# Kernel optimization log

Measured on AMD Instinct MI355X. Metric: run time of the kernel, lower is better.

## Reference

```python
import math
import jax, jax.numpy as jnp
import numpy as np

SAMPLE_RATE = 16000
N_BANDS = 3
_F_DARK = jnp.array([270.0, 800.0, 2300.0], dtype=jnp.float32)
_F_NEUTRAL = jnp.array([500.0, 1500.0, 2500.0], dtype=jnp.float32)
_F_BRIGHT = jnp.array([730.0, 2100.0, 3000.0], dtype=jnp.float32)
_Q_DARK = jnp.array([5.0, 5.0, 5.0], dtype=jnp.float32)
_Q_NEUTRAL = jnp.array([8.0, 8.0, 8.0], dtype=jnp.float32)
_Q_BRIGHT = jnp.array([12.0, 12.0, 12.0], dtype=jnp.float32)


def _interpolate_formants(level):
    # level: [B] in [0,1] -> freqs, qs: [B, n_bands]
    t_low = jnp.clip(level * 2.0, 0.0, 1.0)[:, None]
    t_high = jnp.clip((level - 0.5) * 2.0, 0.0, 1.0)[:, None]
    use_high = (level >= 0.5)[:, None]
    freqs_lo = (1.0 - t_low) * _F_DARK + t_low * _F_NEUTRAL
    qs_lo = (1.0 - t_low) * _Q_DARK + t_low * _Q_NEUTRAL
    freqs_hi = (1.0 - t_high) * _F_NEUTRAL + t_high * _F_BRIGHT
    qs_hi = (1.0 - t_high) * _Q_NEUTRAL + t_high * _Q_BRIGHT
    freqs = jnp.where(use_high, freqs_hi, freqs_lo)
    qs = jnp.where(use_high, qs_hi, qs_lo)
    return freqs, qs


def _biquad_bandpass_coeffs(freq_hz, q):
    # freq_hz, q: [B, n_bands] -> coeffs each [B, n_bands]; b1 is 0
    omega = (2.0 * math.pi / SAMPLE_RATE) * freq_hz
    sin_o = jnp.sin(omega)
    cos_o = jnp.cos(omega)
    alpha = sin_o / (2.0 * jnp.maximum(q, 0.5))
    a0 = 1.0 + alpha
    b0 = alpha / a0
    b2 = -alpha / a0
    a1 = (-2.0 * cos_o) / a0
    a2 = (1.0 - alpha) / a0
    return b0, b2, a1, a2


def setup_inputs() -> dict:
    key = jax.random.key(0)
    k1, k2 = jax.random.split(key)
    B, S = 256, 131072
    audio = jax.random.normal(k1, (B, S), dtype=jnp.float32)
    resonance_level = jax.random.uniform(k2, (B,), dtype=jnp.float32)
    return {"audio": audio, "resonance_level": resonance_level}


def reference(audio, resonance_level):
    B, S = audio.shape
    level = jnp.clip(resonance_level.astype(audio.dtype), 0.0, 1.0)
    freqs, qs = _interpolate_formants(level)          # [B, nb]
    b0, b2, a1, a2 = _biquad_bandpass_coeffs(freqs, qs)
    # broadcast coeffs to [nb, B] for the scan
    b0, b2, a1, a2 = (c.T for c in (b0, b2, a1, a2))
    nb = N_BANDS
    zeros = jnp.zeros((nb, B), dtype=audio.dtype)
    inv_sqrt_nb = 1.0 / math.sqrt(nb)

    def step(carry, x_t):
        # carry: (x1, x2, y1, y2) each [nb, B]; x_t: [B]
        x1, x2, y1, y2 = carry
        y = b0 * x_t[None, :] + b2 * x2 - a1 * y1 - a2 * y2  # [nb, B]
        new_x1 = jnp.broadcast_to(x_t[None, :], (nb, B))
        return (new_x1, x1, y, y1), jnp.sum(y, axis=0) * inv_sqrt_nb

    _, out = jax.lax.scan(step, (zeros, zeros, zeros, zeros), audio.T)  # out: [S, B]
    return out.T
```

## Files before the change

kernel.cpp:

```cpp
#include <hip/hip_runtime.h>
#include <math.h>

#ifndef M_PI
#define M_PI 3.14159265358979323846
#endif

#define BATCHES 256
#define S_LEN   131072

#define TPB   320
#define MAINT 256
#define CCH   16
#define SEGS  32
#define SEG_SAMPS (MAINT * CCH)
#define WCH   48
#define NCH   (MAINT + WCH)
#define OBSTR 17
#define SCAN_OFF 4352
#define SCAN_STR 305
#define H_OFF 6184
#define LDSF  6232

typedef float v4f __attribute__((ext_vector_type(4)));

__device__ __forceinline__ void compute_coeffs(float level_in, float b0[3], float na1[3], float na2[3]) {
    const float FD[3] = {270.0f, 800.0f, 2300.0f};
    const float FN[3] = {500.0f, 1500.0f, 2500.0f};
    const float FB[3] = {730.0f, 2100.0f, 3000.0f};
    float level = fminf(fmaxf(level_in, 0.0f), 1.0f);
    float t_low  = fminf(fmaxf(level * 2.0f, 0.0f), 1.0f);
    float t_high = fminf(fmaxf((level - 0.5f) * 2.0f, 0.0f), 1.0f);
    bool hi = (level >= 0.5f);
    const float W0 = (float)(2.0 * M_PI / 16000.0);
    #pragma unroll
    for (int k = 0; k < 3; ++k) {
        float f, q;
        if (hi) { f = (1.0f - t_high) * FN[k] + t_high * FB[k];
                  q = (1.0f - t_high) * 8.0f  + t_high * 12.0f; }
        else    { f = (1.0f - t_low) * FD[k] + t_low * FN[k];
                  q = (1.0f - t_low) * 5.0f  + t_low * 8.0f; }
        float omega = W0 * f;
        float sn = __sinf(omega), cs = __cosf(omega);
        float alpha = sn / (2.0f * fmaxf(q, 0.5f));
        float a0 = 1.0f + alpha;
        b0[k]  = alpha / a0;
        na1[k] = (2.0f * cs) / a0;
        na2[k] = -((1.0f - alpha) / a0);
    }
}

#define STEP3(XT, XTM2, SUMV)                                                    \
    {                                                                            \
        float d = (XT) - (XTM2);                                                 \
        float e0 = fmaf(b0[0], d, na2[0] * y2[0]);                               \
        float e1 = fmaf(b0[1], d, na2[1] * y2[1]);                               \
        float e2 = fmaf(b0[2], d, na2[2] * y2[2]);                               \
        float yy0 = fmaf(na1[0], y1[0], e0);                                     \
        float yy1 = fmaf(na1[1], y1[1], e1);                                     \
        float yy2 = fmaf(na1[2], y1[2], e2);                                     \
        y2[0] = y1[0]; y1[0] = yy0;                                              \
        y2[1] = y1[1]; y1[1] = yy1;                                              \
        y2[2] = y1[2]; y1[2] = yy2;                                              \
        SUMV = (yy0 + yy1 + yy2);                                                \
    }

#define MMUL(R00,R01,R10,R11, X00,X01,X10,X11, Y00,Y01,Y10,Y11)                  \
    {                                                                            \
        R00 = X00*Y00 + X01*Y10; R01 = X00*Y01 + X01*Y11;                        \
        R10 = X10*Y00 + X11*Y10; R11 = X10*Y01 + X11*Y11;                        \
    }

__global__ __launch_bounds__(TPB, 2)
void formant_onepass(const float* __restrict__ x, const float* __restrict__ lvl,
                     float* __restrict__ out)
{
    __shared__ float lds[LDSF];

    const int tid = threadIdx.x;
    const int row = blockIdx.x >> 5;
    const int seg = blockIdx.x & (SEGS - 1);

    float b0[3], na1[3], na2[3];
    compute_coeffs(lvl[row], b0, na1, na2);

    const float* xrow = x + (size_t)row * S_LEN;
    const size_t segBase = (size_t)seg * SEG_SAMPS;

    if (tid < MAINT) {
        const float* xc = xrow + segBase + (size_t)tid * CCH;
        float xm1 = 0.f, xm2 = 0.f;
        if (seg > 0 || tid > 0) { float2 t2 = *(const float2*)(xc - 2); xm2 = t2.x; xm1 = t2.y; }
        float y1[3] = {0.f,0.f,0.f}, y2[3] = {0.f,0.f,0.f};
        const float4* xv = (const float4*)xc;
        float* myob = lds + tid * OBSTR;
        float4 buf[4];
        #pragma unroll
        for (int j = 0; j < 4; ++j) buf[j] = xv[j];
        #pragma unroll
        for (int i = 0; i < 4; ++i) {
            float4 q = buf[i];
            float4 o;
            STEP3(q.x, xm2, o.x)
            STEP3(q.y, xm1, o.y)
            STEP3(q.z, q.x, o.z)
            STEP3(q.w, q.y, o.w)
            xm2 = q.z; xm1 = q.w;
            myob[4*i + 0] = o.x;
            myob[4*i + 1] = o.y;
            myob[4*i + 2] = o.z;
            myob[4*i + 3] = o.w;
        }
        lds[SCAN_OFF + 0*SCAN_STR + WCH + tid] = y1[0];
        lds[SCAN_OFF + 1*SCAN_STR + WCH + tid] = y2[0];
        lds[SCAN_OFF + 2*SCAN_STR + WCH + tid] = y1[1];
        lds[SCAN_OFF + 3*SCAN_STR + WCH + tid] = y2[1];
        lds[SCAN_OFF + 4*SCAN_STR + WCH + tid] = y1[2];
        lds[SCAN_OFF + 5*SCAN_STR + WCH + tid] = y2[2];
    }
    else if (tid < MAINT + WCH) {
        const int wid = tid - MAINT;
        if (seg == 0) {
            #pragma unroll
            for (int e = 0; e < 6; ++e) lds[SCAN_OFF + e*SCAN_STR + wid] = 0.f;
        } else {
            const float* xw = xrow + segBase - (size_t)(WCH * CCH) + (size_t)wid * CCH;
            float2 t2 = *(const float2*)(xw - 2);
            float y1[3] = {0.f,0.f,0.f}, y2[3] = {0.f,0.f,0.f};
            float p2 = t2.x, p1 = t2.y, dummy;
            const float4* xv = (const float4*)xw;
            float4 buf[4];
            #pragma unroll
            for (int j = 0; j < 4; ++j) buf[j] = xv[j];
            #pragma unroll
            for (int i = 0; i < 4; ++i) {
                float4 q = buf[i];
                STEP3(q.x, p2, dummy)
                STEP3(q.y, p1, dummy)
                STEP3(q.z, q.x, dummy)
                STEP3(q.w, q.y, dummy)
                p2 = q.z; p1 = q.w;
            }
            (void)dummy;
            lds[SCAN_OFF + 0*SCAN_STR + wid] = y1[0];
            lds[SCAN_OFF + 1*SCAN_STR + wid] = y2[0];
            lds[SCAN_OFF + 2*SCAN_STR + wid] = y1[1];
            lds[SCAN_OFF + 3*SCAN_STR + wid] = y2[1];
            lds[SCAN_OFF + 4*SCAN_STR + wid] = y1[2];
            lds[SCAN_OFF + 5*SCAN_STR + wid] = y2[2];
        }
    }
    __syncthreads();

    {
        const int wv = tid >> 6, ln = tid & 63;
        if (wv < 3) {
            const float A1 = na1[wv], A2 = na2[wv];
            float hm1 = 1.f, hm2 = 0.f, hm3 = 0.f;
            for (int i = 0; i < CCH; ++i) {
                float h = fmaf(A1, hm1, A2 * hm2);
                hm3 = hm2; hm2 = hm1; hm1 = h;
                if (ln == 0) lds[H_OFF + wv * CCH + i] = h;
            }
            const float H00 = hm1, H01 = A2 * hm2;
            const float H10 = hm2, H11 = A2 * hm3;

            float* z1p = lds + SCAN_OFF + (2*wv) * SCAN_STR;
            float* z2p = lds + SCAN_OFF + (2*wv + 1) * SCAN_STR;

            const int cnt = (ln < 48) ? 5 : 4;
            const int beg = (ln < 48) ? 5 * ln : 240 + 4 * (ln - 48);

            float s1 = 0.f, s2 = 0.f;
            for (int j = 0; j < cnt; ++j) {
                float z1 = z1p[beg + j], z2 = z2p[beg + j];
                float n1 = z1 + H00 * s1 + H01 * s2;
                float n2 = z2 + H10 * s1 + H11 * s2;
                s1 = n1; s2 = n2;
            }
            float B00,B01,B10,B11, C00,C01,C10,C11;
            MMUL(B00,B01,B10,B11, H00,H01,H10,H11, H00,H01,H10,H11)
            MMUL(C00,C01,C10,C11, B00,B01,B10,B11, B00,B01,B10,B11)
            float A00 = C00, A01 = C01, A10 = C10, A11 = C11;
            if (cnt == 5) {
                float D00,D01,D10,D11;
                MMUL(D00,D01,D10,D11, C00,C01,C10,C11, H00,H01,H10,H11)
                A00 = D00; A01 = D01; A10 = D10; A11 = D11;
            }
            float bb1 = s1, bb2 = s2;
            for (int d = 1; d < 64; d <<= 1) {
                float iA00 = __shfl_up(A00, d), iA01 = __shfl_up(A01, d);
                float iA10 = __shfl_up(A10, d), iA11 = __shfl_up(A11, d);
                float ib1  = __shfl_up(bb1, d), ib2  = __shfl_up(bb2, d);
                if (ln >= d) {
                    float nb1 = A00 * ib1 + A01 * ib2 + bb1;
                    float nb2 = A10 * ib1 + A11 * ib2 + bb2;
                    float n00, n01, n10, n11;
                    MMUL(n00,n01,n10,n11, A00,A01,A10,A11, iA00,iA01,iA10,iA11)
                    A00 = n00; A01 = n01; A10 = n10; A11 = n11;
                    bb1 = nb1; bb2 = nb2;
                }
            }
            float e1 = __shfl_up(bb1, 1), e2 = __shfl_up(bb2, 1);
            if (ln == 0) { e1 = 0.f; e2 = 0.f; }

            s1 = e1; s2 = e2;
            for (int j = 0; j < cnt; ++j) {
                int w = beg + j;
                float z1 = z1p[w], z2 = z2p[w];
                z1p[w] = s1; z2p[w] = s2;
                float n1 = z1 + H00 * s1 + H01 * s2;
                float n2 = z2 + H10 * s1 + H11 * s2;
                s1 = n1; s2 = n2;
            }
        }
    }
    __syncthreads();

    {
        const float is3 = 0.57735026918962576f;
        float* obase = out + (size_t)row * S_LEN + segBase;

#define EMIT_OUT(F)                                                              \
        {                                                                        \
            const int f   = (F);                                                 \
            const int ch  = f >> 2;                                              \
            const int off = f & 3;                                               \
            const int t   = off * 4;                                             \
            const float* sp = lds + ch * OBSTR + t;                              \
            float o0 = sp[0], o1 = sp[1], o2 = sp[2], o3 = sp[3];                \
            _Pragma("unroll")                                                    \
            for (int k = 0; k < 3; ++k) {                                        \
                const float c1 = lds[SCAN_OFF + (2*k)   * SCAN_STR + WCH + ch];  \
                const float c2 = na2[k] *                                        \
                    lds[SCAN_OFF + (2*k+1) * SCAN_STR + WCH + ch];               \
                const float4 hv = *(const float4*)&lds[H_OFF + k * CCH + t];     \
                const float hm = (off == 0) ? 1.0f : lds[H_OFF + k*CCH + t - 1]; \
                o0 = fmaf(c1, hv.x, fmaf(c2, hm,   o0));                         \
                o1 = fmaf(c1, hv.y, fmaf(c2, hv.x, o1));                         \
                o2 = fmaf(c1, hv.z, fmaf(c2, hv.y, o2));                         \
                o3 = fmaf(c1, hv.w, fmaf(c2, hv.z, o3));                         \
            }                                                                    \
            v4f o = { o0 * is3, o1 * is3, o2 * is3, o3 * is3 };                  \
            __builtin_nontemporal_store(o, (v4f*)(obase + (size_t)f * 4));       \
        }

        #pragma unroll
        for (int j = 0; j < 3; ++j)
            EMIT_OUT(j * TPB + tid)
        if (tid < 1024 - 3 * TPB)
            EMIT_OUT(3 * TPB + tid)
#undef EMIT_OUT
    }
}

extern "C" void kernel_launch(void* const* d_in, const int* in_sizes, int n_in,
                              void* d_out, int out_size, void* d_ws, size_t ws_size,
                              hipStream_t stream) {
    const float* audio = (const float*)d_in[0];
    const float* level = (const float*)d_in[1];
    float* out = (float*)d_out;
    (void)in_sizes; (void)n_in; (void)d_ws; (void)ws_size; (void)out_size;

    formant_onepass<<<BATCHES * SEGS, TPB, 0, stream>>>(audio, level, out);
}
```

Before: 58.00 us.

## Keep zero-state outputs in registers and apply carry correction before LDS transpose

```diff
diff --git a/kernel.cpp b/kernel.cpp
--- a/kernel.cpp
+++ b/kernel.cpp
@@ -14,12 +14,10 @@
 #define SEGS  32
 #define SEG_SAMPS (MAINT * CCH)
 #define WCH   48
-#define NCH   (MAINT + WCH)
-#define OBSTR 17
-#define SCAN_OFF 4352
+#define OBSTR 20
 #define SCAN_STR 305
-#define H_OFF 6184
-#define LDSF  6232
+#define H_OFF 5120
+#define LDSF  (H_OFF + 3 * CCH)
 
 typedef float v4f __attribute__((ext_vector_type(4)));
 
@@ -86,13 +84,14 @@
     const float* xrow = x + (size_t)row * S_LEN;
     const size_t segBase = (size_t)seg * SEG_SAMPS;
 
+    float4 szs[4];
+
     if (tid < MAINT) {
         const float* xc = xrow + segBase + (size_t)tid * CCH;
         float xm1 = 0.f, xm2 = 0.f;
         if (seg > 0 || tid > 0) { float2 t2 = *(const float2*)(xc - 2); xm2 = t2.x; xm1 = t2.y; }
         float y1[3] = {0.f,0.f,0.f}, y2[3] = {0.f,0.f,0.f};
         const float4* xv = (const float4*)xc;
-        float* myob = lds + tid * OBSTR;
         float4 buf[4];
         #pragma unroll
         for (int j = 0; j < 4; ++j) buf[j] = xv[j];
@@ -105,23 +104,20 @@
             STEP3(q.z, q.x, o.z)
             STEP3(q.w, q.y, o.w)
             xm2 = q.z; xm1 = q.w;
-            myob[4*i + 0] = o.x;
-            myob[4*i + 1] = o.y;
-            myob[4*i + 2] = o.z;
-            myob[4*i + 3] = o.w;
-        }
-        lds[SCAN_OFF + 0*SCAN_STR + WCH + tid] = y1[0];
-        lds[SCAN_OFF + 1*SCAN_STR + WCH + tid] = y2[0];
-        lds[SCAN_OFF + 2*SCAN_STR + WCH + tid] = y1[1];
-        lds[SCAN_OFF + 3*SCAN_STR + WCH + tid] = y2[1];
-        lds[SCAN_OFF + 4*SCAN_STR + WCH + tid] = y1[2];
-        lds[SCAN_OFF + 5*SCAN_STR + WCH + tid] = y2[2];
+            szs[i] = o;
+        }
+        lds[0*SCAN_STR + WCH + tid] = y1[0];
+        lds[1*SCAN_STR + WCH + tid] = y2[0];
+        lds[2*SCAN_STR + WCH + tid] = y1[1];
+        lds[3*SCAN_STR + WCH + tid] = y2[1];
+        lds[4*SCAN_STR + WCH + tid] = y1[2];
+        lds[5*SCAN_STR + WCH + tid] = y2[2];
     }
     else if (tid < MAINT + WCH) {
         const int wid = tid - MAINT;
         if (seg == 0) {
             #pragma unroll
-            for (int e = 0; e < 6; ++e) lds[SCAN_OFF + e*SCAN_STR + wid] = 0.f;
+            for (int e = 0; e < 6; ++e) lds[e*SCAN_STR + wid] = 0.f;
         } else {
             const float* xw = xrow + segBase - (size_t)(WCH * CCH) + (size_t)wid * CCH;
             float2 t2 = *(const float2*)(xw - 2);
@@ -141,12 +137,12 @@
                 p2 = q.z; p1 = q.w;
             }
             (void)dummy;
-            lds[SCAN_OFF + 0*SCAN_STR + wid] = y1[0];
-            lds[SCAN_OFF + 1*SCAN_STR + wid] = y2[0];
-            lds[SCAN_OFF + 2*SCAN_STR + wid] = y1[1];
-            lds[SCAN_OFF + 3*SCAN_STR + wid] = y2[1];
-            lds[SCAN_OFF + 4*SCAN_STR + wid] = y1[2];
-            lds[SCAN_OFF + 5*SCAN_STR + wid] = y2[2];
+            lds[0*SCAN_STR + wid] = y1[0];
+            lds[1*SCAN_STR + wid] = y2[0];
+            lds[2*SCAN_STR + wid] = y1[1];
+            lds[3*SCAN_STR + wid] = y2[1];
+            lds[4*SCAN_STR + wid] = y1[2];
+            lds[5*SCAN_STR + wid] = y2[2];
         }
     }
     __syncthreads();
@@ -164,8 +160,8 @@
             const float H00 = hm1, H01 = A2 * hm2;
             const float H10 = hm2, H11 = A2 * hm3;
 
-            float* z1p = lds + SCAN_OFF + (2*wv) * SCAN_STR;
-            float* z2p = lds + SCAN_OFF + (2*wv + 1) * SCAN_STR;
+            float* z1p = lds + (2*wv) * SCAN_STR;
+            float* z2p = lds + (2*wv + 1) * SCAN_STR;
 
             const int cnt = (ln < 48) ? 5 : 4;
             const int beg = (ln < 48) ? 5 * ln : 240 + 4 * (ln - 48);
@@ -216,40 +212,52 @@
     }
     __syncthreads();
 
+    float c1k[3], c2k[3];
+    if (tid < MAINT) {
+        #pragma unroll
+        for (int k = 0; k < 3; ++k) {
+            c1k[k] = lds[(2*k) * SCAN_STR + WCH + tid];
+            c2k[k] = na2[k] * lds[(2*k + 1) * SCAN_STR + WCH + tid];
+        }
+    }
+    __syncthreads();
+
+    if (tid < MAINT) {
+        const float is3 = 0.57735026918962576f;
+        float* myst = lds + tid * OBSTR;
+        float hp[3] = {1.f, 1.f, 1.f};
+        #pragma unroll
+        for (int i = 0; i < 4; ++i) {
+            float4 s = szs[i];
+            float o0 = s.x, o1 = s.y, o2 = s.z, o3 = s.w;
+            #pragma unroll
+            for (int k = 0; k < 3; ++k) {
+                const float4 hv = *(const float4*)&lds[H_OFF + k * CCH + 4 * i];
+                o0 = fmaf(c1k[k], hv.x, fmaf(c2k[k], hp[k], o0));
+                o1 = fmaf(c1k[k], hv.y, fmaf(c2k[k], hv.x,  o1));
+                o2 = fmaf(c1k[k], hv.z, fmaf(c2k[k], hv.y,  o2));
+                o3 = fmaf(c1k[k], hv.w, fmaf(c2k[k], hv.z,  o3));
+                hp[k] = hv.w;
+            }
+            v4f o = { o0 * is3, o1 * is3, o2 * is3, o3 * is3 };
+            *(v4f*)(myst + 4 * i) = o;
+        }
+    }
+    __syncthreads();
+
     {
-        const float is3 = 0.57735026918962576f;
         float* obase = out + (size_t)row * S_LEN + segBase;
-
-#define EMIT_OUT(F)                                                              \
-        {                                                                        \
-            const int f   = (F);                                                 \
-            const int ch  = f >> 2;                                              \
-            const int off = f & 3;                                               \
-            const int t   = off * 4;                                             \
-            const float* sp = lds + ch * OBSTR + t;                              \
-            float o0 = sp[0], o1 = sp[1], o2 = sp[2], o3 = sp[3];                \
-            _Pragma("unroll")                                                    \
-            for (int k = 0; k < 3; ++k) {                                        \
-                const float c1 = lds[SCAN_OFF + (2*k)   * SCAN_STR + WCH + ch];  \
-                const float c2 = na2[k] *                                        \
-                    lds[SCAN_OFF + (2*k+1) * SCAN_STR + WCH + ch];               \
-                const float4 hv = *(const float4*)&lds[H_OFF + k * CCH + t];     \
-                const float hm = (off == 0) ? 1.0f : lds[H_OFF + k*CCH + t - 1]; \
-                o0 = fmaf(c1, hv.x, fmaf(c2, hm,   o0));                         \
-                o1 = fmaf(c1, hv.y, fmaf(c2, hv.x, o1));                         \
-                o2 = fmaf(c1, hv.z, fmaf(c2, hv.y, o2));                         \
-                o3 = fmaf(c1, hv.w, fmaf(c2, hv.z, o3));                         \
-            }                                                                    \
-            v4f o = { o0 * is3, o1 * is3, o2 * is3, o3 * is3 };                  \
-            __builtin_nontemporal_store(o, (v4f*)(obase + (size_t)f * 4));       \
-        }
-
-        #pragma unroll
-        for (int j = 0; j < 3; ++j)
-            EMIT_OUT(j * TPB + tid)
-        if (tid < 1024 - 3 * TPB)
-            EMIT_OUT(3 * TPB + tid)
-#undef EMIT_OUT
+        #pragma unroll
+        for (int j = 0; j < 3; ++j) {
+            const int f = j * TPB + tid;
+            const v4f o = *(const v4f*)(lds + (f >> 2) * OBSTR + (f & 3) * 4);
+            __builtin_nontemporal_store(o, (v4f*)(obase + (size_t)f * 4));
+        }
+        if (tid < 1024 - 3 * TPB) {
+            const int f = 3 * TPB + tid;
+            const v4f o = *(const v4f*)(lds + (f >> 2) * OBSTR + (f & 3) * 4);
+            __builtin_nontemporal_store(o, (v4f*)(obase + (size_t)f * 4));
+        }
     }
 }
 
```

Result: no change. 57.53 us (median of 2 runs) (-0.8%).
